# Performance work log

Hardware: AMD Instinct MI355X
Metric: run time of the kernel (lower is better)

The kernel has to match this reference:

```python
import jax, jax.numpy as jnp
import numpy as np

B = 32; IMG = 224; P = 16; D = 768; NH = 12; HD = 64; L = 12; MLP = 3072; S0 = 197
NE = 10; LP = 40; NPL = 5; NC = 100; EPS = 1e-6
POS_PROMPT = (0, 1, 2, 3, 4)


def setup_inputs() -> dict:
    ks = jax.random.split(jax.random.key(0), 18)
    n = lambda k, shp: jax.random.normal(k, shp, jnp.float32) * 0.02
    return {
        "inputs": jax.random.normal(ks[0], (B, 3, IMG, IMG), jnp.float32),
        "expert_ids": jax.random.randint(ks[1], (B,), 0, NE),
        "patch_w": n(ks[2], (D, 3, P, P)),
        "patch_b": n(ks[3], (D,)),
        "cls_token": n(ks[4], (1, 1, D)),
        "pos_embed": n(ks[5], (1, S0, D)),
        "ln1_s": jnp.ones((L, D), jnp.float32),
        "ln1_b": jnp.zeros((L, D), jnp.float32),
        "qkv_w": n(ks[6], (L, D, 3 * D)),
        "qkv_b": n(ks[7], (L, 3 * D)),
        "proj_w": n(ks[8], (L, D, D)),
        "proj_b": n(ks[9], (L, D)),
        "ln2_s": jnp.ones((L, D), jnp.float32),
        "ln2_b": jnp.zeros((L, D), jnp.float32),
        "fc1_w": n(ks[10], (L, D, MLP)),
        "fc1_b": n(ks[11], (L, MLP)),
        "fc2_w": n(ks[12], (L, MLP, D)),
        "fc2_b": n(ks[13], (L, D)),
        "norm_s": jnp.ones((D,), jnp.float32),
        "norm_b": jnp.zeros((D,), jnp.float32),
        "prompts": jax.random.uniform(ks[14], (NPL, NE, LP, D), jnp.float32),
        "head_w": n(ks[15], (NE, D, NC)),
        "head_b": n(ks[16], (NE, NC)),
    }


def _ln(x, s, b):
    m = x.mean(-1, keepdims=True)
    v = ((x - m) ** 2).mean(-1, keepdims=True)
    return (x - m) * jax.lax.rsqrt(v + EPS) * s + b


def _forward(inputs, expert_ids, patch_w, patch_b, cls_token, pos_embed,
             ln1_s, ln1_b, qkv_w, qkv_b, proj_w, proj_b, ln2_s, ln2_b,
             fc1_w, fc1_b, fc2_w, fc2_b, norm_s, norm_b, prompts, head_w, head_b):
    # patch embed: conv stride 16 -> [B, D, 14, 14] -> [B, 196, D]
    x = jax.lax.conv_general_dilated(inputs, patch_w, (P, P), 'VALID',
                                     dimension_numbers=('NCHW', 'OIHW', 'NCHW'))
    x = x.reshape(B, D, -1).transpose(0, 2, 1) + patch_b
    x = jnp.concatenate([jnp.broadcast_to(cls_token, (B, 1, D)), x], axis=1) + pos_embed
    # per-sample expert prompt gather: [B, NPL, LP, D], plus cls pos bias
    bp = jnp.take(prompts, expert_ids, axis=1).transpose(1, 0, 2, 3) + pos_embed[0, 0]
    scale = 1.0 / np.sqrt(HD)
    for i in range(L):
        if i in POS_PROMPT:
            x = jnp.concatenate([x, bp[:, POS_PROMPT.index(i)]], axis=1)
        S = x.shape[1]
        h = _ln(x, ln1_s[i], ln1_b[i])
        qkv = (h @ qkv_w[i] + qkv_b[i]).reshape(B, S, 3, NH, HD).transpose(2, 0, 3, 1, 4)
        q, k, v = qkv[0], qkv[1], qkv[2]
        att = jax.nn.softmax(jnp.einsum('bhqd,bhkd->bhqk', q, k) * scale, axis=-1)
        o = jnp.einsum('bhqk,bhkd->bhqd', att, v).transpose(0, 2, 1, 3).reshape(B, S, D)
        x = x + o @ proj_w[i] + proj_b[i]
        h = _ln(x, ln2_s[i], ln2_b[i])
        x = x + jax.nn.gelu(h @ fc1_w[i] + fc1_b[i], approximate=False) @ fc2_w[i] + fc2_b[i]
        x = x[:, :S0]  # drop prompt tokens after each block
    feat = _ln(x, norm_s, norm_b)[:, 0]
    # per-sample expert head dispatch: gathered-weight batched matvec
    return jnp.einsum('bd,bdc->bc', feat, head_w[expert_ids]) + head_b[expert_ids]


def reference(inputs, expert_ids, patch_w, patch_b, cls_token, pos_embed,
              ln1_s, ln1_b, qkv_w, qkv_b, proj_w, proj_b, ln2_s, ln2_b,
              fc1_w, fc1_b, fc2_w, fc2_b, norm_s, norm_b, prompts, head_w, head_b):
    return _forward(inputs, expert_ids, patch_w, patch_b, cls_token, pos_embed,
                    ln1_s, ln1_b, qkv_w, qkv_b, proj_w, proj_b, ln2_s, ln2_b,
                    fc1_w, fc1_b, fc2_w, fc2_b, norm_s, norm_b, prompts, head_w, head_b)
```

## Files before the change

kernel.cpp:

```cpp
#include <hip/hip_runtime.h>

typedef unsigned short ushort_t;
typedef __attribute__((ext_vector_type(8))) short short8;
typedef __attribute__((ext_vector_type(4))) float floatx4;

#define D_    768
#define SMAX  237
#define S0_   197
#define RPAD  7680
#define NHEAD 12
#define BATCH 32

__device__ __forceinline__ ushort_t f2bf(float f) {
  union { float f; unsigned u; } v; v.f = f;
  unsigned r = v.u + 0x7FFFu + ((v.u >> 16) & 1u);
  return (ushort_t)(r >> 16);
}
__device__ __forceinline__ float bf2f(ushort_t u) {
  union { unsigned u; float f; } v; v.u = ((unsigned)u) << 16; return v.f;
}
__device__ __forceinline__ void async16(const void* g, void* l) {
  __builtin_amdgcn_global_load_lds((const __attribute__((address_space(1))) void*)g,
                                   (__attribute__((address_space(3))) void*)l, 16, 0, 0);
}

__global__ __launch_bounds__(256) void patchify_kernel(
    const float* __restrict__ in, ushort_t* __restrict__ Xp) {
  int rowid = blockIdx.x;
  int b = rowid / 196, p = rowid - b * 196;
  int py = p / 14, px = p - py * 14;
  int tid = threadIdx.x;
#pragma unroll
  for (int t = 0; t < 3; ++t) {
    int k = tid + t * 256;
    int c = k >> 8, rem = k & 255, i = rem >> 4, j = rem & 15;
    float v = in[(((size_t)b * 3 + c) * 224 + py * 16 + i) * 224 + px * 16 + j];
    Xp[(size_t)rowid * 768 + k] = f2bf(v);
  }
}

__global__ void cvt_bf16_kernel(const float* __restrict__ src, ushort_t* __restrict__ dst, int n) {
  int i = blockIdx.x * 256 + threadIdx.x;
  if (i < n) dst[i] = f2bf(src[i]);
}

__global__ void cls_fill_kernel(const float* __restrict__ cls, const float* __restrict__ pos,
                                float* __restrict__ X) {
  int b = blockIdx.x, d = threadIdx.x;
  X[(size_t)(b * SMAX) * 768 + d] = cls[d] + pos[d];
}

__global__ void prompt_fill_kernel(const float* __restrict__ prompts, const float* __restrict__ pos,
                                   const int* __restrict__ eid, float* __restrict__ X, int layer) {
  int id = blockIdx.x;
  int b = id / 40, p = id - b * 40;
  int e = eid[b];
  float v = prompts[(((size_t)layer * 10 + e) * 40 + p) * 768 + threadIdx.x] + pos[threadIdx.x];
  X[((size_t)b * SMAX + 197 + p) * 768 + threadIdx.x] = v;
}

__global__ __launch_bounds__(256) void transpose_wts_kernel(
    const float* __restrict__ qkvw, const float* __restrict__ projw,
    const float* __restrict__ fc1w, const float* __restrict__ fc2w,
    ushort_t* __restrict__ wq, ushort_t* __restrict__ wp,
    ushort_t* __restrict__ w1, ushort_t* __restrict__ w2) {
  int id = blockIdx.x;
  const float* src; ushort_t* dst; int K, N, t;
  if (id < 1728)      { src = qkvw; dst = wq; K = 768;  N = 2304; t = id; }
  else if (id < 2304) { src = projw; dst = wp; K = 768;  N = 768;  t = id - 1728; }
  else if (id < 4608) { src = fc1w; dst = w1; K = 768;  N = 3072; t = id - 2304; }
  else                { src = fc2w; dst = w2; K = 3072; N = 768;  t = id - 4608; }
  int ntn = N >> 5;
  int k0 = (t / ntn) * 32, n0 = (t % ntn) * 32;
  __shared__ float tile[32][33];
  int tx = threadIdx.x & 31, ty = threadIdx.x >> 5;
#pragma unroll
  for (int q = 0; q < 4; ++q) {
    int kk = q * 8 + ty;
    tile[kk][tx] = src[(size_t)(k0 + kk) * N + n0 + tx];
  }
  __syncthreads();
#pragma unroll
  for (int q = 0; q < 4; ++q) {
    int nn = q * 8 + ty;
    dst[(size_t)(n0 + nn) * K + k0 + tx] = f2bf(tile[tx][nn]);
  }
}

__global__ __launch_bounds__(256) void ln_kernel(
    const float* __restrict__ X, const float* __restrict__ s, const float* __restrict__ bt,
    ushort_t* __restrict__ H) {
  int row = blockIdx.x, tid = threadIdx.x;
  const float* xr = X + (size_t)row * 768;
  float v0 = xr[tid], v1 = xr[tid + 256], v2 = xr[tid + 512];
  float sum = v0 + v1 + v2;
  float sq = v0 * v0 + v1 * v1 + v2 * v2;
#pragma unroll
  for (int off = 32; off; off >>= 1) {
    sum += __shfl_down(sum, off, 64);
    sq  += __shfl_down(sq,  off, 64);
  }
  __shared__ float red[8];
  int wv = tid >> 6, ln = tid & 63;
  if (ln == 0) { red[wv] = sum; red[4 + wv] = sq; }
  __syncthreads();
  if (tid == 0) {
    red[0] = red[0] + red[1] + red[2] + red[3];
    red[4] = red[4] + red[5] + red[6] + red[7];
  }
  __syncthreads();
  float mean = red[0] * (1.f / 768.f);
  float var  = red[4] * (1.f / 768.f) - mean * mean;
  float rs = rsqrtf(var + 1e-6f);
  ushort_t* hr = H + (size_t)row * 768;
  hr[tid]       = f2bf((v0 - mean) * rs * s[tid]       + bt[tid]);
  hr[tid + 256] = f2bf((v1 - mean) * rs * s[tid + 256] + bt[tid + 256]);
  hr[tid + 512] = f2bf((v2 - mean) * rs * s[tid + 512] + bt[tid + 512]);
}

enum { EPI_BF16 = 0, EPI_GELU = 1, EPI_RESID = 2, EPI_PATCH = 3 };

template <int EPI>
__global__ __launch_bounds__(256) void gemm_kernel(
    const ushort_t* __restrict__ A, int lda,
    const ushort_t* __restrict__ BT,
    const float* __restrict__ bias,
    float* __restrict__ XO, ushort_t* __restrict__ O,
    const float* __restrict__ pos,
    int N, int K) {
  __shared__ ushort_t As[128 * 32];
  __shared__ ushort_t Bs[128 * 32];
  int m0 = blockIdx.y * 128, n0 = blockIdx.x * 128;
  int tid = threadIdx.x, lane = tid & 63, wv = tid >> 6;
  int wm = (wv >> 1) * 64, wn = (wv & 1) * 64;
  int fr = lane & 15, kg = lane >> 4;
  int sw = (kg ^ ((fr >> 1) & 3)) * 8;

  floatx4 acc[4][4];
#pragma unroll
  for (int i = 0; i < 4; ++i)
#pragma unroll
    for (int j = 0; j < 4; ++j) acc[i][j] = (floatx4){0.f, 0.f, 0.f, 0.f};

  for (int k0 = 0; k0 < K; k0 += 32) {
#pragma unroll
    for (int t = 0; t < 2; ++t) {
      int flat = (wv * 2 + t) * 64 + lane;
      int row = flat >> 2;
      int ch = ((flat & 3) ^ ((flat >> 3) & 3)) * 8;
      async16(A + (size_t)(m0 + row) * lda + k0 + ch, &As[(wv * 2 + t) * 512]);
      async16(BT + (size_t)(n0 + row) * K + k0 + ch, &Bs[(wv * 2 + t) * 512]);
    }
    __syncthreads();
    short8 af[4], bfr[4];
#pragma unroll
    for (int i = 0; i < 4; ++i) af[i] = *(const short8*)&As[(wm + i * 16 + fr) * 32 + sw];
#pragma unroll
    for (int j = 0; j < 4; ++j) bfr[j] = *(const short8*)&Bs[(wn + j * 16 + fr) * 32 + sw];
#pragma unroll
    for (int i = 0; i < 4; ++i)
#pragma unroll
      for (int j = 0; j < 4; ++j)
        acc[i][j] = __builtin_amdgcn_mfma_f32_16x16x32_bf16(af[i], bfr[j], acc[i][j], 0, 0, 0);
    __syncthreads();
  }

  int rbase = (lane >> 4) * 4;
#pragma unroll
  for (int i = 0; i < 4; ++i) {
#pragma unroll
    for (int j = 0; j < 4; ++j) {
      int col = n0 + wn + j * 16 + fr;
#pragma unroll
      for (int r = 0; r < 4; ++r) {
        int row = m0 + wm + i * 16 + rbase + r;
        float v = acc[i][j][r] + bias[col];
        if (EPI == EPI_BF16) {
          O[(size_t)row * N + col] = f2bf(v);
        } else if (EPI == EPI_GELU) {
          float g = 0.5f * v * (1.0f + erff(v * 0.70710678118f));
          O[(size_t)row * N + col] = f2bf(g);
        } else if (EPI == EPI_RESID) {
          XO[(size_t)row * 768 + col] += v;
        } else {
          int b = row / 196, p = row - b * 196;
          int orow = b * SMAX + 1 + p;
          XO[(size_t)orow * 768 + col] = v + pos[(size_t)(1 + p) * 768 + col];
        }
      }
    }
  }
}

__global__ __launch_bounds__(256) void attn_kernel(ushort_t* __restrict__ qkv, int S) {
  __shared__ ushort_t Kc[64 * 64];
  __shared__ ushort_t Vt[64 * 72];
  __shared__ ushort_t Pb[4][16 * 72];
  int id = blockIdx.x;
  int qc = id & 3, bh = id >> 2;
  int b = bh / NHEAD, h = bh - b * NHEAD;
  size_t rowbase = (size_t)b * SMAX;
  int tid = threadIdx.x, lane = tid & 63, wv = tid >> 6;
  int fr = lane & 15, kg = lane >> 4;
  int q0 = qc * 64 + wv * 16;

  const ushort_t* qp = qkv + (rowbase + q0 + fr) * 2304 + h * 64 + kg * 8;
  short8 qf0 = *(const short8*)qp;
  short8 qf1 = *(const short8*)(qp + 32);

  floatx4 oacc[4];
#pragma unroll
  for (int j = 0; j < 4; ++j) oacc[j] = (floatx4){0.f, 0.f, 0.f, 0.f};
  float lsum[4] = {0.f, 0.f, 0.f, 0.f};

  int ksw = kg ^ (fr & 7);
  int kst_g = (lane & 7) ^ ((lane >> 3) & 7);

  for (int c = 0; c < 4; ++c) {
    int key0 = c * 64;
    __syncthreads();
#pragma unroll
    for (int t = 0; t < 2; ++t) {
      int f = (wv * 2 + t) * 64 + lane;
      int krow = f >> 3;
      async16(qkv + (rowbase + key0 + krow) * 2304 + 768 + h * 64 + kst_g * 8,
              &Kc[(wv * 2 + t) * 512]);
    }
#pragma unroll
    for (int t = 0; t < 2; ++t) {
      int kc = wv * 2 + t;
      short8 vv = *(const short8*)(qkv + (rowbase + key0 + lane) * 2304 + 1536 + h * 64 + kc * 8);
#pragma unroll
      for (int e = 0; e < 8; ++e) Vt[(kc * 8 + e) * 72 + lane] = (ushort_t)vv[e];
    }
    __syncthreads();

    floatx4 sacc[4];
#pragma unroll
    for (int j = 0; j < 4; ++j) sacc[j] = (floatx4){0.f, 0.f, 0.f, 0.f};
#pragma unroll
    for (int j = 0; j < 4; ++j) {
      int krow = j * 16 + fr;
      short8 b0 = *(const short8*)&Kc[krow * 64 + ksw * 8];
      short8 b1 = *(const short8*)&Kc[krow * 64 + (ksw ^ 4) * 8];
      sacc[j] = __builtin_amdgcn_mfma_f32_16x16x32_bf16(qf0, b0, sacc[j], 0, 0, 0);
      sacc[j] = __builtin_amdgcn_mfma_f32_16x16x32_bf16(qf1, b1, sacc[j], 0, 0, 0);
    }

#pragma unroll
    for (int j = 0; j < 4; ++j) {
      int key = key0 + j * 16 + fr;
      bool valid = key < S;
#pragma unroll
      for (int r = 0; r < 4; ++r) {
        float e = valid ? __expf(sacc[j][r] * 0.125f) : 0.f;
        lsum[r] += e;
        Pb[wv][(kg * 4 + r) * 72 + j * 16 + fr] = f2bf(e);
      }
    }
    __syncthreads();

    const ushort_t* pp = &Pb[wv][fr * 72 + kg * 8];
    short8 p0 = *(const short8*)pp;
    short8 p1 = *(const short8*)(pp + 32);
#pragma unroll
    for (int j = 0; j < 4; ++j) {
      const ushort_t* vp = &Vt[(j * 16 + fr) * 72 + kg * 8];
      short8 v0 = *(const short8*)vp;
      short8 v1 = *(const short8*)(vp + 32);
      oacc[j] = __builtin_amdgcn_mfma_f32_16x16x32_bf16(p0, v0, oacc[j], 0, 0, 0);
      oacc[j] = __builtin_amdgcn_mfma_f32_16x16x32_bf16(p1, v1, oacc[j], 0, 0, 0);
    }
  }

#pragma unroll
  for (int r = 0; r < 4; ++r) {
#pragma unroll
    for (int m = 1; m <= 8; m <<= 1) lsum[r] += __shfl_xor(lsum[r], m, 64);
  }
#pragma unroll
  for (int r = 0; r < 4; ++r) {
    int q = q0 + kg * 4 + r;
    if (q < S) {
      float inv = 1.f / lsum[r];
      ushort_t* op = qkv + (rowbase + q) * 2304 + h * 64;
#pragma unroll
      for (int j = 0; j < 4; ++j) op[j * 16 + fr] = f2bf(oacc[j][r] * inv);
    }
  }
}

__global__ __launch_bounds__(256) void head_kernel(
    const float* __restrict__ X, const float* __restrict__ ns, const float* __restrict__ nb,
    const int* __restrict__ eid, const float* __restrict__ hw, const float* __restrict__ hb,
    float* __restrict__ out) {
  int b = blockIdx.x, tid = threadIdx.x;
  const float* xr = X + (size_t)(b * SMAX) * 768;
  float v0 = xr[tid], v1 = xr[tid + 256], v2 = xr[tid + 512];
  float sum = v0 + v1 + v2;
  float sq = v0 * v0 + v1 * v1 + v2 * v2;
#pragma unroll
  for (int off = 32; off; off >>= 1) {
    sum += __shfl_down(sum, off, 64);
    sq  += __shfl_down(sq,  off, 64);
  }
  __shared__ float red[8];
  __shared__ float feat[768];
  int wv = tid >> 6, ln = tid & 63;
  if (ln == 0) { red[wv] = sum; red[4 + wv] = sq; }
  __syncthreads();
  if (tid == 0) {
    red[0] = red[0] + red[1] + red[2] + red[3];
    red[4] = red[4] + red[5] + red[6] + red[7];
  }
  __syncthreads();
  float mean = red[0] * (1.f / 768.f);
  float var  = red[4] * (1.f / 768.f) - mean * mean;
  float rs = rsqrtf(var + 1e-6f);
  feat[tid]       = (v0 - mean) * rs * ns[tid]       + nb[tid];
  feat[tid + 256] = (v1 - mean) * rs * ns[tid + 256] + nb[tid + 256];
  feat[tid + 512] = (v2 - mean) * rs * ns[tid + 512] + nb[tid + 512];
  __syncthreads();
  int e = eid[b];
  if (tid < 100) {
    float a = hb[e * 100 + tid];
    const float* w = hw + (size_t)e * 768 * 100 + tid;
#pragma unroll 4
    for (int d = 0; d < 768; ++d) a += feat[d] * w[(size_t)d * 100];
    out[b * 100 + tid] = a;
  }
}

extern "C" void kernel_launch(void* const* d_in, const int* in_sizes, int n_in,
                              void* d_out, int out_size, void* d_ws, size_t ws_size,
                              hipStream_t stream) {
  const float* inputs     = (const float*)d_in[0];
  const int*   expert_ids = (const int*)d_in[1];
  const float* patch_w    = (const float*)d_in[2];
  const float* patch_b    = (const float*)d_in[3];
  const float* cls_token  = (const float*)d_in[4];
  const float* pos_embed  = (const float*)d_in[5];
  const float* ln1_s      = (const float*)d_in[6];
  const float* ln1_b      = (const float*)d_in[7];
  const float* qkv_w      = (const float*)d_in[8];
  const float* qkv_b      = (const float*)d_in[9];
  const float* proj_w     = (const float*)d_in[10];
  const float* proj_b     = (const float*)d_in[11];
  const float* ln2_s      = (const float*)d_in[12];
  const float* ln2_b      = (const float*)d_in[13];
  const float* fc1_w      = (const float*)d_in[14];
  const float* fc1_b      = (const float*)d_in[15];
  const float* fc2_w      = (const float*)d_in[16];
  const float* fc2_b      = (const float*)d_in[17];
  const float* norm_s     = (const float*)d_in[18];
  const float* norm_b     = (const float*)d_in[19];
  const float* prompts    = (const float*)d_in[20];
  const float* head_w     = (const float*)d_in[21];
  const float* head_b     = (const float*)d_in[22];
  float* out = (float*)d_out;

  char* ws = (char*)d_ws;
  size_t off = 0;
  ushort_t* WTp = (ushort_t*)(ws + off); off += (size_t)768 * 768 * 2;
  ushort_t* WQ  = (ushort_t*)(ws + off); off += (size_t)2304 * 768 * 2;
  ushort_t* WP  = (ushort_t*)(ws + off); off += (size_t)768 * 768 * 2;
  ushort_t* W1  = (ushort_t*)(ws + off); off += (size_t)3072 * 768 * 2;
  ushort_t* W2  = (ushort_t*)(ws + off); off += (size_t)768 * 3072 * 2;
  float*    X   = (float*)(ws + off);    off += (size_t)RPAD * 768 * 4;
  ushort_t* H   = (ushort_t*)(ws + off); off += (size_t)RPAD * 768 * 2;
  ushort_t* QKV = (ushort_t*)(ws + off); off += (size_t)RPAD * 2304 * 2;
  ushort_t* MID = (ushort_t*)(ws + off); off += (size_t)RPAD * 3072 * 2;
  ushort_t* XP  = MID;

  cvt_bf16_kernel<<<(768 * 768 + 255) / 256, 256, 0, stream>>>(patch_w, WTp, 768 * 768);
  patchify_kernel<<<6272, 256, 0, stream>>>(inputs, XP);
  gemm_kernel<EPI_PATCH><<<dim3(6, 49), 256, 0, stream>>>(
      XP, 768, WTp, patch_b, X, nullptr, pos_embed, 768, 768);
  cls_fill_kernel<<<BATCH, 768, 0, stream>>>(cls_token, pos_embed, X);

  for (int i = 0; i < 12; ++i) {
    int S = (i < 5) ? SMAX : S0_;
    if (i < 5)
      prompt_fill_kernel<<<BATCH * 40, 768, 0, stream>>>(prompts, pos_embed, expert_ids, X, i);
    transpose_wts_kernel<<<6912, 256, 0, stream>>>(
        qkv_w + (size_t)i * 768 * 2304, proj_w + (size_t)i * 768 * 768,
        fc1_w + (size_t)i * 768 * 3072, fc2_w + (size_t)i * 3072 * 768,
        WQ, WP, W1, W2);
    ln_kernel<<<RPAD, 256, 0, stream>>>(X, ln1_s + i * 768, ln1_b + i * 768, H);
    gemm_kernel<EPI_BF16><<<dim3(18, 60), 256, 0, stream>>>(
        H, 768, WQ, qkv_b + i * 2304, nullptr, QKV, nullptr, 2304, 768);
    attn_kernel<<<BATCH * NHEAD * 4, 256, 0, stream>>>(QKV, S);
    gemm_kernel<EPI_RESID><<<dim3(6, 60), 256, 0, stream>>>(
        QKV, 2304, WP, proj_b + i * 768, X, nullptr, nullptr, 768, 768);
    ln_kernel<<<RPAD, 256, 0, stream>>>(X, ln2_s + i * 768, ln2_b + i * 768, H);
    gemm_kernel<EPI_GELU><<<dim3(24, 60), 256, 0, stream>>>(
        H, 768, W1, fc1_b + i * 3072, nullptr, MID, nullptr, 3072, 768);
    gemm_kernel<EPI_RESID><<<dim3(6, 60), 256, 0, stream>>>(
        MID, 3072, W2, fc2_b + i * 768, X, nullptr, nullptr, 768, 3072);
  }

  head_kernel<<<BATCH, 256, 0, stream>>>(X, norm_s, norm_b, expert_ids, head_w, head_b, out);
}
```

Measured before the change: 3.612 ms.

## Switch to token-major layout, shrink rows after prompts, split-K residual GEMMs

Reorders the activation buffer from batch-major to token-major (row = token*32 + batch). Once the prompt tokens are dropped, only the first 197*32 rows stay live, so LN and the GEMMs after layer 5 cover 50 M-tiles instead of 60. The residual GEMMs (proj, fc2) split K in two and accumulate with atomicAdd to get more blocks. The GEMM grid is also flattened and remapped in an XCD-aware interleave. Attention clamps key/query rows to S-1. The costs are atomic traffic, non-deterministic summation order, and GEMM tiles that read stale padding rows.

```diff
diff --git a/kernel.cpp b/kernel.cpp
--- a/kernel.cpp
+++ b/kernel.cpp
@@ -11,6 +11,7 @@
 #define NHEAD 12
 #define BATCH 32
 
+
 __device__ __forceinline__ ushort_t f2bf(float f) {
   union { float f; unsigned u; } v; v.f = f;
   unsigned r = v.u + 0x7FFFu + ((v.u >> 16) & 1u);
@@ -47,7 +48,7 @@
 __global__ void cls_fill_kernel(const float* __restrict__ cls, const float* __restrict__ pos,
                                 float* __restrict__ X) {
   int b = blockIdx.x, d = threadIdx.x;
-  X[(size_t)(b * SMAX) * 768 + d] = cls[d] + pos[d];
+  X[(size_t)b * 768 + d] = cls[d] + pos[d];
 }
 
 __global__ void prompt_fill_kernel(const float* __restrict__ prompts, const float* __restrict__ pos,
@@ -56,7 +57,7 @@
   int b = id / 40, p = id - b * 40;
   int e = eid[b];
   float v = prompts[(((size_t)layer * 10 + e) * 40 + p) * 768 + threadIdx.x] + pos[threadIdx.x];
-  X[((size_t)b * SMAX + 197 + p) * 768 + threadIdx.x] = v;
+  X[((size_t)(197 + p) * 32 + b) * 768 + threadIdx.x] = v;
 }
 
 __global__ __launch_bounds__(256) void transpose_wts_kernel(
@@ -123,14 +124,22 @@
 template <int EPI>
 __global__ __launch_bounds__(256) void gemm_kernel(
     const ushort_t* __restrict__ A, int lda,
-    const ushort_t* __restrict__ BT,
+    const ushort_t* __restrict__ BT, int ldb,
     const float* __restrict__ bias,
     float* __restrict__ XO, ushort_t* __restrict__ O,
     const float* __restrict__ pos,
-    int N, int K) {
+    int N, int nx, int my, int Klen, int nt) {
   __shared__ ushort_t As[128 * 32];
   __shared__ ushort_t Bs[128 * 32];
-  int m0 = blockIdx.y * 128, n0 = blockIdx.x * 128;
+  int per = gridDim.x >> 3;
+  int F = blockIdx.x;
+  int T = (F & 7) * per + (F >> 3);
+  if (T >= nt) return;
+  int n_i = T % nx, rest = T / nx;
+  int m_i = rest % my, kz = rest / my;
+  int m0 = m_i * 128, n0 = n_i * 128;
+  int kb = kz * Klen, ke = kb + Klen;
+
   int tid = threadIdx.x, lane = tid & 63, wv = tid >> 6;
   int wm = (wv >> 1) * 64, wn = (wv & 1) * 64;
   int fr = lane & 15, kg = lane >> 4;
@@ -142,14 +151,14 @@
 #pragma unroll
     for (int j = 0; j < 4; ++j) acc[i][j] = (floatx4){0.f, 0.f, 0.f, 0.f};
 
-  for (int k0 = 0; k0 < K; k0 += 32) {
+  for (int k0 = kb; k0 < ke; k0 += 32) {
 #pragma unroll
     for (int t = 0; t < 2; ++t) {
       int flat = (wv * 2 + t) * 64 + lane;
       int row = flat >> 2;
       int ch = ((flat & 3) ^ ((flat >> 3) & 3)) * 8;
       async16(A + (size_t)(m0 + row) * lda + k0 + ch, &As[(wv * 2 + t) * 512]);
-      async16(BT + (size_t)(n0 + row) * K + k0 + ch, &Bs[(wv * 2 + t) * 512]);
+      async16(BT + (size_t)(n0 + row) * ldb + k0 + ch, &Bs[(wv * 2 + t) * 512]);
     }
     __syncthreads();
     short8 af[4], bfr[4];
@@ -174,18 +183,19 @@
 #pragma unroll
       for (int r = 0; r < 4; ++r) {
         int row = m0 + wm + i * 16 + rbase + r;
-        float v = acc[i][j][r] + bias[col];
         if (EPI == EPI_BF16) {
-          O[(size_t)row * N + col] = f2bf(v);
+          O[(size_t)row * N + col] = f2bf(acc[i][j][r] + bias[col]);
         } else if (EPI == EPI_GELU) {
+          float v = acc[i][j][r] + bias[col];
           float g = 0.5f * v * (1.0f + erff(v * 0.70710678118f));
           O[(size_t)row * N + col] = f2bf(g);
         } else if (EPI == EPI_RESID) {
-          XO[(size_t)row * 768 + col] += v;
+          float v = acc[i][j][r] + (kz == 0 ? bias[col] : 0.f);
+          atomicAdd(&XO[(size_t)row * 768 + col], v);
         } else {
           int b = row / 196, p = row - b * 196;
-          int orow = b * SMAX + 1 + p;
-          XO[(size_t)orow * 768 + col] = v + pos[(size_t)(1 + p) * 768 + col];
+          size_t orow = (size_t)(1 + p) * 32 + b;
+          XO[orow * 768 + col] = acc[i][j][r] + bias[col] + pos[(size_t)(1 + p) * 768 + col];
         }
       }
     }
@@ -199,12 +209,12 @@
   int id = blockIdx.x;
   int qc = id & 3, bh = id >> 2;
   int b = bh / NHEAD, h = bh - b * NHEAD;
-  size_t rowbase = (size_t)b * SMAX;
   int tid = threadIdx.x, lane = tid & 63, wv = tid >> 6;
   int fr = lane & 15, kg = lane >> 4;
   int q0 = qc * 64 + wv * 16;
 
-  const ushort_t* qp = qkv + (rowbase + q0 + fr) * 2304 + h * 64 + kg * 8;
+  int qr = q0 + fr; if (qr > S - 1) qr = S - 1;
+  const ushort_t* qp = qkv + ((size_t)qr * 32 + b) * 2304 + h * 64 + kg * 8;
   short8 qf0 = *(const short8*)qp;
   short8 qf1 = *(const short8*)(qp + 32);
 
@@ -222,14 +232,15 @@
 #pragma unroll
     for (int t = 0; t < 2; ++t) {
       int f = (wv * 2 + t) * 64 + lane;
-      int krow = f >> 3;
-      async16(qkv + (rowbase + key0 + krow) * 2304 + 768 + h * 64 + kst_g * 8,
+      int kr = key0 + (f >> 3); if (kr > S - 1) kr = S - 1;
+      async16(qkv + ((size_t)kr * 32 + b) * 2304 + 768 + h * 64 + kst_g * 8,
               &Kc[(wv * 2 + t) * 512]);
     }
 #pragma unroll
     for (int t = 0; t < 2; ++t) {
       int kc = wv * 2 + t;
-      short8 vv = *(const short8*)(qkv + (rowbase + key0 + lane) * 2304 + 1536 + h * 64 + kc * 8);
+      int vr = key0 + lane; if (vr > S - 1) vr = S - 1;
+      short8 vv = *(const short8*)(qkv + ((size_t)vr * 32 + b) * 2304 + 1536 + h * 64 + kc * 8);
 #pragma unroll
       for (int e = 0; e < 8; ++e) Vt[(kc * 8 + e) * 72 + lane] = (ushort_t)vv[e];
     }
@@ -283,7 +294,7 @@
     int q = q0 + kg * 4 + r;
     if (q < S) {
       float inv = 1.f / lsum[r];
-      ushort_t* op = qkv + (rowbase + q) * 2304 + h * 64;
+      ushort_t* op = qkv + ((size_t)q * 32 + b) * 2304 + h * 64;
 #pragma unroll
       for (int j = 0; j < 4; ++j) op[j * 16 + fr] = f2bf(oacc[j][r] * inv);
     }
@@ -295,7 +306,7 @@
     const int* __restrict__ eid, const float* __restrict__ hw, const float* __restrict__ hb,
     float* __restrict__ out) {
   int b = blockIdx.x, tid = threadIdx.x;
-  const float* xr = X + (size_t)(b * SMAX) * 768;
+  const float* xr = X + (size_t)b * 768;
   float v0 = xr[tid], v1 = xr[tid + 256], v2 = xr[tid + 512];
   float sum = v0 + v1 + v2;
   float sq = v0 * v0 + v1 * v1 + v2 * v2;
@@ -374,29 +385,45 @@
 
   cvt_bf16_kernel<<<(768 * 768 + 255) / 256, 256, 0, stream>>>(patch_w, WTp, 768 * 768);
   patchify_kernel<<<6272, 256, 0, stream>>>(inputs, XP);
-  gemm_kernel<EPI_PATCH><<<dim3(6, 49), 256, 0, stream>>>(
-      XP, 768, WTp, patch_b, X, nullptr, pos_embed, 768, 768);
+  {
+    int nt = 6 * 49, ntp = ((nt + 7) / 8) * 8;
+    gemm_kernel<EPI_PATCH><<<ntp, 256, 0, stream>>>(
+        XP, 768, WTp, 768, patch_b, X, nullptr, pos_embed, 768, 6, 49, 768, nt);
+  }
   cls_fill_kernel<<<BATCH, 768, 0, stream>>>(cls_token, pos_embed, X);
 
   for (int i = 0; i < 12; ++i) {
     int S = (i < 5) ? SMAX : S0_;
+    int MT = (i < 5) ? 60 : 50;
     if (i < 5)
       prompt_fill_kernel<<<BATCH * 40, 768, 0, stream>>>(prompts, pos_embed, expert_ids, X, i);
     transpose_wts_kernel<<<6912, 256, 0, stream>>>(
         qkv_w + (size_t)i * 768 * 2304, proj_w + (size_t)i * 768 * 768,
         fc1_w + (size_t)i * 768 * 3072, fc2_w + (size_t)i * 3072 * 768,
         WQ, WP, W1, W2);
-    ln_kernel<<<RPAD, 256, 0, stream>>>(X, ln1_s + i * 768, ln1_b + i * 768, H);
-    gemm_kernel<EPI_BF16><<<dim3(18, 60), 256, 0, stream>>>(
-        H, 768, WQ, qkv_b + i * 2304, nullptr, QKV, nullptr, 2304, 768);
+    ln_kernel<<<MT * 128, 256, 0, stream>>>(X, ln1_s + i * 768, ln1_b + i * 768, H);
+    {
+      int nt = 18 * MT;
+      gemm_kernel<EPI_BF16><<<nt, 256, 0, stream>>>(
+          H, 768, WQ, 768, qkv_b + i * 2304, nullptr, QKV, nullptr, 2304, 18, MT, 768, nt);
+    }
     attn_kernel<<<BATCH * NHEAD * 4, 256, 0, stream>>>(QKV, S);
-    gemm_kernel<EPI_RESID><<<dim3(6, 60), 256, 0, stream>>>(
-        QKV, 2304, WP, proj_b + i * 768, X, nullptr, nullptr, 768, 768);
-    ln_kernel<<<RPAD, 256, 0, stream>>>(X, ln2_s + i * 768, ln2_b + i * 768, H);
-    gemm_kernel<EPI_GELU><<<dim3(24, 60), 256, 0, stream>>>(
-        H, 768, W1, fc1_b + i * 3072, nullptr, MID, nullptr, 3072, 768);
-    gemm_kernel<EPI_RESID><<<dim3(6, 60), 256, 0, stream>>>(
-        MID, 3072, W2, fc2_b + i * 768, X, nullptr, nullptr, 768, 3072);
+    {
+      int nt = 6 * MT * 2;
+      gemm_kernel<EPI_RESID><<<nt, 256, 0, stream>>>(
+          QKV, 2304, WP, 768, proj_b + i * 768, X, nullptr, nullptr, 768, 6, MT, 384, nt);
+    }
+    ln_kernel<<<MT * 128, 256, 0, stream>>>(X, ln2_s + i * 768, ln2_b + i * 768, H);
+    {
+      int nt = 24 * MT;
+      gemm_kernel<EPI_GELU><<<nt, 256, 0, stream>>>(
+          H, 768, W1, 768, fc1_b + i * 3072, nullptr, MID, nullptr, 3072, 24, MT, 768, nt);
+    }
+    {
+      int nt = 6 * MT * 2;
+      gemm_kernel<EPI_RESID><<<nt, 256, 0, stream>>>(
+          MID, 3072, W2, 3072, fc2_b + i * 768, X, nullptr, nullptr, 768, 6, MT, 1536, nt);
+    }
   }
 
   head_kernel<<<BATCH, 256, 0, stream>>>(X, norm_s, norm_b, expert_ids, head_w, head_b, out);
```

After: 3.834 ms. 6.1% more time.
